# Optimization experiments

Hardware: AMD Instinct MI355X
Metric: run time of the kernel (lower is better)

The kernel has to match this reference:

```python
import jax, jax.numpy as jnp
import numpy as np

TOL_A = 1e-09


def setup_inputs() -> dict:
    key = jax.random.key(0)
    ks = jax.random.split(key, 6)
    nx, nu, ny, bsz, T = 256, 128, 128, 128, 2048
    return {
        "u": jax.random.normal(ks[0], (bsz, T, nu), jnp.float32),
        "M": jax.random.normal(ks[1], (2 * nx, 2 * nx), jnp.float32),
        "B": jax.random.normal(ks[2], (nx, nu), jnp.float32),
        "C": jax.random.normal(ks[3], (ny, nx), jnp.float32),
        "D": jax.random.normal(ks[4], (ny, nu), jnp.float32),
        "x0": jax.random.normal(ks[5], (nx, 1), jnp.float32),
    }


def _compute_A(M):
    # LMI-based stable A: S = M M^T + tol*I; A = E^{-1} F
    nx = M.shape[0] // 2
    S = M @ M.T + TOL_A * jnp.eye(2 * nx, dtype=M.dtype)
    F = S[nx:, :nx]
    P = S[nx:, nx:]
    E = 0.5 * (P + S[:nx, :nx])
    return jnp.linalg.solve(E, F)  # == inv(E) @ F


def reference(u, M, B, C, D, x0):
    # u: (bsz, T, nu); returns predictions (bsz, T, ny)
    nx = B.shape[0]
    A = _compute_A(M)  # time-invariant: computed once instead of per step
    bsz = u.shape[0]
    x = jnp.broadcast_to(x0[:, 0], (bsz, nx))  # learned x0 stacked over batch
    # t=0 output: C x0 + D u_0 (faithful to torch code)
    y0 = x @ C.T + u[:, 0] @ D.T

    def step(x, u_t):
        # x_{t+1} = A x_t + B u_t ; y_{t+1} = C x_{t+1} + D u_t (off-by-one D term, as in source)
        x = x @ A.T + u_t @ B.T
        y = x @ C.T + u_t @ D.T
        return x, y

    # scan over time: xs is (T-1, bsz, nu)
    _, ys = jax.lax.scan(step, x, jnp.swapaxes(u[:, :-1], 0, 1))
    preds = jnp.concatenate([y0[None], ys], axis=0)  # (T, bsz, ny)
    return jnp.swapaxes(preds, 0, 1)
```

## Files before the change

kernel.cpp:

```cpp
#include <hip/hip_runtime.h>

#define NX 256
#define NU 128
#define NY 128
#define BSZ 128
#define TT 2048
#define LCH 32
#define KCH 64

typedef _Float16 h8 __attribute__((ext_vector_type(8)));
typedef _Float16 h4 __attribute__((ext_vector_type(4)));
typedef float f4 __attribute__((ext_vector_type(4)));

__device__ __forceinline__ f4 mfma16(h8 a, h8 b, f4 c) {
  return __builtin_amdgcn_mfma_f32_16x16x32_f16(a, b, c, 0, 0, 0);
}
#define PIN(x) asm volatile("" : "+v"(x))
#define LBAR() asm volatile("s_waitcnt lgkmcnt(0)\n\ts_barrier" ::: "memory")

__device__ __forceinline__ int swz256(int row, int bc) { return row * 256 + (bc ^ ((row & 7) << 4)); }

__device__ __forceinline__ h8 cvt8(f4 lo, f4 hi) {
  h8 h;
#pragma unroll
  for (int j = 0; j < 4; ++j) { h[j] = (_Float16)lo[j]; h[j + 4] = (_Float16)hi[j]; }
  return h;
}
__device__ __forceinline__ h4 h4cvt(f4 v) {
  h4 h;
#pragma unroll
  for (int j = 0; j < 4; ++j) h[j] = (_Float16)v[j];
  return h;
}
__device__ __forceinline__ h8 h8zero() {
  h8 h;
#pragma unroll
  for (int j = 0; j < 8; ++j) h[j] = (_Float16)0.0f;
  return h;
}

__device__ __forceinline__ void mm_core(const float* __restrict__ a, const float* __restrict__ b,
                                        int Nb, int i0, int j0, int tid,
                                        float (*As)[32][65], float (*Bs)[64][33],
                                        float acc[2][2]) {
  const int ar = tid >> 4, ac = (tid & 15) * 4;
  const int br = tid >> 3, bc = (tid & 7) * 4;
  const int tx = tid & 15, ty = tid >> 4;
  f4 pa0 = *(const f4*)(a + (size_t)(i0 + ar) * 256 + ac);
  f4 pa1 = *(const f4*)(a + (size_t)(i0 + ar + 16) * 256 + ac);
  f4 pb0 = *(const f4*)(b + (size_t)br * Nb + j0 + bc);
  f4 pb1 = *(const f4*)(b + (size_t)(br + 32) * Nb + j0 + bc);
  for (int r4 = 0; r4 < 4; ++r4) {
    const int bs = r4 & 1;
#pragma unroll
    for (int m = 0; m < 4; ++m) {
      As[bs][ar][ac + m] = pa0[m];
      As[bs][ar + 16][ac + m] = pa1[m];
      Bs[bs][br][bc + m] = pb0[m];
      Bs[bs][br + 32][bc + m] = pb1[m];
    }
    if (r4 < 3) {
      int kk = (r4 + 1) * 64;
      pa0 = *(const f4*)(a + (size_t)(i0 + ar) * 256 + kk + ac);
      pa1 = *(const f4*)(a + (size_t)(i0 + ar + 16) * 256 + kk + ac);
      pb0 = *(const f4*)(b + (size_t)(kk + br) * Nb + j0 + bc);
      pb1 = *(const f4*)(b + (size_t)(kk + br + 32) * Nb + j0 + bc);
    }
    __syncthreads();
#pragma unroll 8
    for (int k = 0; k < 64; ++k) {
      float a0 = As[bs][ty * 2][k], a1 = As[bs][ty * 2 + 1][k];
      float b0 = Bs[bs][k][tx * 2], b1 = Bs[bs][k][tx * 2 + 1];
      acc[0][0] += a0 * b0; acc[0][1] += a0 * b1;
      acc[1][0] += a1 * b0; acc[1][1] += a1 * b1;
    }
  }
}

__global__ __launch_bounds__(256) void k_ef(const float* __restrict__ M, const float* __restrict__ B,
                                            const float* __restrict__ C, const float* __restrict__ D,
                                            const float* __restrict__ x0, const float* __restrict__ u,
                                            float* __restrict__ E, float* __restrict__ F,
                                            _Float16* __restrict__ B16, float* __restrict__ out) {
  const int tid = threadIdx.x;
  int z = blockIdx.x >> 6;
  if (z >= 2) {
    if (blockIdx.x < 192) {
      int idx = (blockIdx.x - 128) * 256 + tid;
      int b = idx >> 7, col = idx & 127;
      const float* crow = C + (size_t)col * 256;
      const float* drow = D + (size_t)col * 128;
      const float* ur = u + (size_t)b * (TT * NU);
      float s = 0.f;
#pragma unroll 8
      for (int j = 0; j < 256; j += 4) {
        f4 cv = *(const f4*)(crow + j);
        f4 xv = *(const f4*)(x0 + j);
        s += cv[0] * xv[0] + cv[1] * xv[1] + cv[2] * xv[2] + cv[3] * xv[3];
      }
#pragma unroll 8
      for (int j = 0; j < 128; j += 4) {
        f4 dv = *(const f4*)(drow + j);
        f4 uv = *(const f4*)(ur + j);
        s += dv[0] * uv[0] + dv[1] * uv[1] + dv[2] * uv[2] + dv[3] * uv[3];
      }
      out[(size_t)b * (TT * NY) + col] = s;
    } else {
      int i = (blockIdx.x - 192) * 1024 + tid;
      B16[i] = (_Float16)B[i];
      B16[i + 256] = (_Float16)B[i + 256];
      B16[i + 512] = (_Float16)B[i + 512];
      B16[i + 768] = (_Float16)B[i + 768];
    }
    return;
  }
  __shared__ float Ps[2][32][65], Qs[2][32][65];
  int tile = blockIdx.x & 63;
  int i0 = (tile >> 3) * 32, j0 = (tile & 7) * 32;
  const int ar = tid >> 4, ac = (tid & 15) * 4;
  const int tx = tid & 15, ty = tid >> 4;
  float acc[2][2] = {{0.f, 0.f}, {0.f, 0.f}};
  int np = (z == 0) ? 2 : 1;
  int rc = 0;
  for (int p = 0; p < np; ++p) {
    int po = (z == 0) ? p * 256 : 256;
    int qo = (z == 0) ? p * 256 : 0;
    f4 p0 = *(const f4*)(M + (size_t)(i0 + po + ar) * 512 + ac);
    f4 p1 = *(const f4*)(M + (size_t)(i0 + po + ar + 16) * 512 + ac);
    f4 q0 = *(const f4*)(M + (size_t)(j0 + qo + ar) * 512 + ac);
    f4 q1 = *(const f4*)(M + (size_t)(j0 + qo + ar + 16) * 512 + ac);
    for (int kk = 0; kk < 512; kk += 64) {
      const int bs = rc & 1;
      ++rc;
#pragma unroll
      for (int m = 0; m < 4; ++m) {
        Ps[bs][ar][ac + m] = p0[m];
        Ps[bs][ar + 16][ac + m] = p1[m];
        Qs[bs][ar][ac + m] = q0[m];
        Qs[bs][ar + 16][ac + m] = q1[m];
      }
      if (kk < 448) {
        int k2 = kk + 64;
        p0 = *(const f4*)(M + (size_t)(i0 + po + ar) * 512 + k2 + ac);
        p1 = *(const f4*)(M + (size_t)(i0 + po + ar + 16) * 512 + k2 + ac);
        q0 = *(const f4*)(M + (size_t)(j0 + qo + ar) * 512 + k2 + ac);
// ... 55 lines not shown
    }
    red[tid] = s * s;
  }
  __syncthreads();
  for (int o = 128; o > 0; o >>= 1) { if (tid < o) red[tid] += red[tid + o]; __syncthreads(); }
  float c = sqrtf(n1 / red[0]);
  __syncthreads();
  if (blockIdx.x < 64) {
    int i0 = (blockIdx.x >> 3) * 32, j0 = (blockIdx.x & 7) * 32;
    float acc[2][2] = {{0.f, 0.f}, {0.f, 0.f}};
    mm_core(E, E, 256, i0, j0, tid, As, Bs, acc);
    int tx = tid & 15, ty = tid >> 4;
#pragma unroll
    for (int ii = 0; ii < 2; ++ii)
#pragma unroll
      for (int jj = 0; jj < 2; ++jj) {
        int i = i0 + ty * 2 + ii, j = j0 + tx * 2 + jj;
        Y[(size_t)i * 256 + j] = 2.f * c * E[(size_t)i * 256 + j] - c * c * acc[ii][jj];
      }
  } else {
    int idx = (blockIdx.x - 64) * 1024 + tid * 4;
    int i = idx >> 8, j = idx & 255;
    f4 e = *(const f4*)(E + idx);
    f4 v;
#pragma unroll
    for (int m = 0; m < 4; ++m) v[m] = ((j + m) == i ? 2.f * c : 0.f) - c * c * e[m];
    *(f4*)(X + idx) = v;
  }
}

struct MMJob {
  const float* a; const float* b; const float* add;
  float* d32; _Float16* d16;
  int M, N, mode, blk0;
};

__global__ __launch_bounds__(256) void k_mm(MMJob j0, MMJob j1, MMJob j2, int njobs) {
  __shared__ float As[2][32][65];
  __shared__ float Bs[2][64][33];
  const int tid = threadIdx.x;
  int bid = blockIdx.x;
  MMJob jb = j0;
  if (njobs > 1 && bid >= j1.blk0) jb = j1;
  if (njobs > 2 && bid >= j2.blk0) jb = j2;
  int rel = bid - jb.blk0;
  int ntile = jb.N >> 5;
  int i0 = (rel / ntile) * 32, j0g = (rel % ntile) * 32;
  float acc[2][2] = {{0.f, 0.f}, {0.f, 0.f}};
  mm_core(jb.a, jb.b, jb.N, i0, j0g, tid, As, Bs, acc);
  int tx = tid & 15, ty = tid >> 4;
#pragma unroll
  for (int ii = 0; ii < 2; ++ii)
#pragma unroll
    for (int jj = 0; jj < 2; ++jj) {
      int i = i0 + ty * 2 + ii, j = j0g + tx * 2 + jj;
      size_t o = (size_t)i * jb.N + j;
      float v = acc[ii][jj];
      if (jb.mode == 1) v = 2.f * jb.a[(size_t)i * 256 + j] - v;
      else if (jb.add) v += jb.add[o];
      if (jb.d32) jb.d32[o] = v;
      if (jb.d16) jb.d16[o] = (_Float16)v;
    }
}

__global__ __launch_bounds__(512, 2) void k_recW(const float* __restrict__ u,
                                                 const _Float16* __restrict__ A16,
                                                 const _Float16* __restrict__ B16,
                                                 float* __restrict__ w) {
  __shared__ __align__(16) char sm[24576];
  char* xb = sm;
  char* ub = sm + 16384;
  const int tid = threadIdx.x, lane = tid & 63, wv = tid >> 6;
  const int g = lane >> 4, lr = lane & 15;
  const int chunk = blockIdx.x >> 3, btile = blockIdx.x & 7;
  const int b0 = btile * 16, t0 = chunk * LCH, nt0 = wv * 2;

  h8 Ar[2][8], Bf[2][4];
#pragma unroll
  for (int n2 = 0; n2 < 2; ++n2) {
#pragma unroll
    for (int kf = 0; kf < 8; ++kf) {
      Ar[n2][kf] = *(const h8*)(A16 + (size_t)((nt0 + n2) * 16 + lr) * NX + kf * 32 + g * 8);
      PIN(Ar[n2][kf]);
    }
#pragma unroll
    for (int kf = 0; kf < 4; ++kf) {
      Bf[n2][kf] = *(const h8*)(B16 + (size_t)((nt0 + n2) * 16 + lr) * NU + kf * 32 + g * 8);
      PIN(Bf[n2][kf]);
    }
  }
  const int urow = tid >> 5, uuc = tid & 31;
  const float* ubase = u + (size_t)(b0 + urow) * (TT * NU) + uuc * 4;
  const int uoff = swz256(urow, uuc * 8);
  {
    f4 r0 = *(const f4*)(ubase + (size_t)t0 * NU);
    *(h4*)(ub + uoff) = h4cvt(r0);
  }
  f4 urA = *(const f4*)(ubase + (size_t)(t0 + 1) * NU);
  f4 urB = *(const f4*)(ubase + (size_t)(t0 + 2 < TT ? t0 + 2 : TT - 1) * NU);
  h8 af[8];
#pragma unroll
  for (int kf = 0; kf < 8; ++kf) af[kf] = h8zero();
  __syncthreads();

  f4 z4 = {0.f, 0.f, 0.f, 0.f};
  f4 xacc[2];
#pragma unroll 2
  for (int i = 0; i < LCH; ++i) {
    const int p = i & 1;
    if (i < LCH - 1) {
      int nt = t0 + i + 3;
      if (nt > TT - 1) nt = TT - 1;
      if (p == 0) {
        *(h4*)(ub + 4096 + uoff) = h4cvt(urA);
        urA = *(const f4*)(ubase + (size_t)nt * NU);
      } else {
        *(h4*)(ub + uoff) = h4cvt(urB);
        urB = *(const f4*)(ubase + (size_t)nt * NU);
      }
    }
    h8 uf[4];
#pragma unroll
    for (int kf = 0; kf < 4; ++kf)
      uf[kf] = *(const h8*)(ub + p * 4096 + swz256(lr, kf * 64 + g * 16));
    __builtin_amdgcn_s_setprio(1);
    xacc[0] = z4; xacc[1] = z4;
#pragma unroll
    for (int kf = 0; kf < 8; ++kf) {
      xacc[0] = mfma16(Ar[0][kf], af[kf], xacc[0]);
      xacc[1] = mfma16(Ar[1][kf], af[kf], xacc[1]);
    }
#pragma unroll
    for (int kf = 0; kf < 4; ++kf) {
      xacc[0] = mfma16(Bf[0][kf], uf[kf], xacc[0]);
      xacc[1] = mfma16(Bf[1][kf], uf[kf], xacc[1]);
    }
    __builtin_amdgcn_s_setprio(0);
    if (i < LCH - 1) {
#pragma unroll
      for (int n2 = 0; n2 < 2; ++n2)
        *(h4*)(xb + (p ^ 1) * 8192 + lr * 512 + ((((nt0 + n2) * 32) + g * 8) ^ ((lr & 7) << 4))) =
            h4cvt(xacc[n2]);
      LBAR();
#pragma unroll
      for (int kf = 0; kf < 8; ++kf)
        af[kf] = *(const h8*)(xb + (p ^ 1) * 8192 + lr * 512 + ((kf * 64 + g * 16) ^ ((lr & 7) << 4)));
    }
  }
#pragma unroll
  for (int n2 = 0; n2 < 2; ++n2)
    *(f4*)(w + ((size_t)chunk * BSZ + b0 + lr) * NX + (nt0 + n2) * 16 + g * 4) = xacc[n2];
}

__global__ __launch_bounds__(512, 2) void k_phB(const float* __restrict__ x0,
                                                const float* __restrict__ w,
                                                const _Float16* __restrict__ Ah16,
                                                float* __restrict__ xs) {
  __shared__ __align__(16) char xb[16384];
  const int tid = threadIdx.x, lane = tid & 63, wv = tid >> 6;
  const int g = lane >> 4, lr = lane & 15;
  const int b0 = blockIdx.x * 16, nt0 = wv * 2;
  h8 Ar[2][8];
#pragma unroll
  for (int n2 = 0; n2 < 2; ++n2)
#pragma unroll
    for (int kf = 0; kf < 8; ++kf) {
      Ar[n2][kf] = *(const h8*)(Ah16 + (size_t)((nt0 + n2) * 16 + lr) * NX + kf * 32 + g * 8);
      PIN(Ar[n2][kf]);
    }
  for (int s = 0; s < 8; ++s) {
    int e = tid + s * 512;
    int row = e >> 8, c = e & 255;
    xs[(size_t)(b0 + row) * NX + c] = x0[c];
  }
  h8 af[8];
#pragma unroll
  for (int kf = 0; kf < 8; ++kf) {
    const float* sp = x0 + kf * 32 + g * 8;
    af[kf] = cvt8(*(const f4*)sp, *(const f4*)(sp + 4));
  }
  f4 wl[2];
#pragma unroll
  for (int n2 = 0; n2 < 2; ++n2)
    wl[n2] = *(const f4*)(w + ((size_t)0 * BSZ + b0 + lr) * NX + (nt0 + n2) * 16 + g * 4);
// ... 2 lines not shown
    const int p = k & 1;
    f4 wn[2] = {z4, z4};
    if (k < KCH - 2) {
#pragma unroll
      for (int n2 = 0; n2 < 2; ++n2)
        wn[n2] = *(const f4*)(w + ((size_t)(k + 1) * BSZ + b0 + lr) * NX + (nt0 + n2) * 16 + g * 4);
    }
    f4 acc[2] = {z4, z4};
#pragma unroll
    for (int kf = 0; kf < 8; ++kf) {
      acc[0] = mfma16(Ar[0][kf], af[kf], acc[0]);
      acc[1] = mfma16(Ar[1][kf], af[kf], acc[1]);
    }
#pragma unroll
    for (int n2 = 0; n2 < 2; ++n2) {
      acc[n2] += wl[n2];
      *(f4*)(xs + ((size_t)(k + 1) * BSZ + b0 + lr) * NX + (nt0 + n2) * 16 + g * 4) = acc[n2];
    }
    if (k < KCH - 2) {
#pragma unroll
      for (int n2 = 0; n2 < 2; ++n2)
        *(h4*)(xb + (p ^ 1) * 8192 + lr * 512 + ((((nt0 + n2) * 32) + g * 8) ^ ((lr & 7) << 4))) =
            h4cvt(acc[n2]);
      LBAR();
#pragma unroll
      for (int kf = 0; kf < 8; ++kf)
        af[kf] = *(const h8*)(xb + (p ^ 1) * 8192 + lr * 512 + ((kf * 64 + g * 16) ^ ((lr & 7) << 4)));
    }
#pragma unroll
    for (int n2 = 0; n2 < 2; ++n2) wl[n2] = wn[n2];
  }
}

__global__ __launch_bounds__(512, 2) void k_recY(const float* __restrict__ u,
                                                 const _Float16* __restrict__ A16,
                                                 const _Float16* __restrict__ B16,
                                                 const _Float16* __restrict__ CA16,
                                                 const _Float16* __restrict__ CBD16,
                                                 const float* __restrict__ xs,
                                                 float* __restrict__ out) {
  __shared__ __align__(16) char sm[24576];
  char* xb = sm;
  char* ub = sm + 16384;
  const int tid = threadIdx.x, lane = tid & 63, wv = tid >> 6;
  const int g = lane >> 4, lr = lane & 15;
  const int chunk = blockIdx.x >> 3, btile = blockIdx.x & 7;
  const int b0 = btile * 16, t0 = chunk * LCH, nt0 = wv * 2;

  h8 Ar[2][8], Bf[2][4], Cf[8], Df[4];
#pragma unroll
  for (int n2 = 0; n2 < 2; ++n2) {
#pragma unroll
    for (int kf = 0; kf < 8; ++kf) {
      Ar[n2][kf] = *(const h8*)(A16 + (size_t)((nt0 + n2) * 16 + lr) * NX + kf * 32 + g * 8);
      PIN(Ar[n2][kf]);
    }
#pragma unroll
    for (int kf = 0; kf < 4; ++kf) {
      Bf[n2][kf] = *(const h8*)(B16 + (size_t)((nt0 + n2) * 16 + lr) * NU + kf * 32 + g * 8);
      PIN(Bf[n2][kf]);
    }
  }
#pragma unroll
  for (int kf = 0; kf < 8; ++kf) {
    Cf[kf] = *(const h8*)(CA16 + (size_t)(wv * 16 + lr) * NX + kf * 32 + g * 8);
    PIN(Cf[kf]);
  }
#pragma unroll
  for (int kf = 0; kf < 4; ++kf) {
    Df[kf] = *(const h8*)(CBD16 + (size_t)(wv * 16 + lr) * NU + kf * 32 + g * 8);
    PIN(Df[kf]);
  }
  h8 af[8];
#pragma unroll
  for (int kf = 0; kf < 8; ++kf) {
    const float* sp = xs + ((size_t)chunk * BSZ + b0 + lr) * NX + kf * 32 + g * 8;
    af[kf] = cvt8(*(const f4*)sp, *(const f4*)(sp + 4));
  }
  const int urow = tid >> 5, uuc = tid & 31;
  const float* ubase = u + (size_t)(b0 + urow) * (TT * NU) + uuc * 4;
  const int uoff = swz256(urow, uuc * 8);
  float* obase = out + (size_t)(b0 + lr) * (TT * NY) + wv * 16 + g * 4;
  {
    f4 r0 = *(const f4*)(ubase + (size_t)t0 * NU);
    *(h4*)(ub + uoff) = h4cvt(r0);
  }
  f4 urA = *(const f4*)(ubase + (size_t)(t0 + 1) * NU);
  f4 urB = *(const f4*)(ubase + (size_t)(t0 + 2 < TT ? t0 + 2 : TT - 1) * NU);
  __syncthreads();

  f4 z4 = {0.f, 0.f, 0.f, 0.f};
#pragma unroll 2
  for (int i = 0; i < LCH; ++i) {
    const int p = i & 1;
    if (i < LCH - 1) {
      int nt = t0 + i + 3;
      if (nt > TT - 1) nt = TT - 1;
      if (p == 0) {
        *(h4*)(ub + 4096 + uoff) = h4cvt(urA);
        urA = *(const f4*)(ubase + (size_t)nt * NU);
      } else {
        *(h4*)(ub + uoff) = h4cvt(urB);
        urB = *(const f4*)(ubase + (size_t)nt * NU);
      }
    }
    h8 uf[4];
#pragma unroll
    for (int kf = 0; kf < 4; ++kf)
      uf[kf] = *(const h8*)(ub + p * 4096 + swz256(lr, kf * 64 + g * 16));
    if (i < LCH - 1) {
      __builtin_amdgcn_s_setprio(1);
      f4 xacc[2] = {z4, z4};
#pragma unroll
      for (int kf = 0; kf < 8; ++kf) {
        xacc[0] = mfma16(Ar[0][kf], af[kf], xacc[0]);
        xacc[1] = mfma16(Ar[1][kf], af[kf], xacc[1]);
      }
#pragma unroll
      for (int kf = 0; kf < 4; ++kf) {
        xacc[0] = mfma16(Bf[0][kf], uf[kf], xacc[0]);
        xacc[1] = mfma16(Bf[1][kf], uf[kf], xacc[1]);
      }
      __builtin_amdgcn_s_setprio(0);
#pragma unroll
      for (int n2 = 0; n2 < 2; ++n2)
        *(h4*)(xb + (p ^ 1) * 8192 + lr * 512 + ((((nt0 + n2) * 32) + g * 8) ^ ((lr & 7) << 4))) =
            h4cvt(xacc[n2]);
    }
    __builtin_amdgcn_s_setprio(1);
    f4 yacc = z4;
#pragma unroll
    for (int kf = 0; kf < 8; ++kf) yacc = mfma16(Cf[kf], af[kf], yacc);
#pragma unroll
    for (int kf = 0; kf < 4; ++kf) yacc = mfma16(Df[kf], uf[kf], yacc);
    __builtin_amdgcn_s_setprio(0);
    int t = t0 + i + 1;
    if (t < TT) *(f4*)(obase + (size_t)t * NY) = yacc;
    if (i < LCH - 1) {
      LBAR();
#pragma unroll
      for (int kf = 0; kf < 8; ++kf)
        af[kf] = *(const h8*)(xb + (p ^ 1) * 8192 + lr * 512 + ((kf * 64 + g * 16) ^ ((lr & 7) << 4)));
    }
  }
}

extern "C" void kernel_launch(void* const* d_in, const int* in_sizes, int n_in,
                              void* d_out, int out_size, void* d_ws, size_t ws_size,
                              hipStream_t stream) {
  const float* u  = (const float*)d_in[0];
  const float* M  = (const float*)d_in[1];
  const float* B  = (const float*)d_in[2];
  const float* C  = (const float*)d_in[3];
  const float* D  = (const float*)d_in[4];
  const float* x0 = (const float*)d_in[5];
  float* out = (float*)d_out;
  char* ws = (char*)d_ws;

  float* E    = (float*)(ws + 0L);
  float* F    = (float*)(ws + 256L * 1024);
  float* X1   = (float*)(ws + 512L * 1024);
  float* Y1   = (float*)(ws + 768L * 1024);
  float* X2   = (float*)(ws + 1024L * 1024);
  float* Y2   = (float*)(ws + 1280L * 1024);
  float* Amat = (float*)(ws + 1536L * 1024);
  float* P2   = (float*)(ws + 1792L * 1024);
  float* P4   = (float*)(ws + 2048L * 1024);
  float* P8   = (float*)(ws + 2304L * 1024);
  float* P16  = (float*)(ws + 2560L * 1024);
  _Float16* A16   = (_Float16*)(ws + 2816L * 1024);
  _Float16* Ah16  = (_Float16*)(ws + 2944L * 1024);
  _Float16* B16   = (_Float16*)(ws + 3072L * 1024);
  _Float16* CA16  = (_Float16*)(ws + 3136L * 1024);
  _Float16* CBD16 = (_Float16*)(ws + 3200L * 1024);
  float* wbuf = (float*)(ws + 9408L * 1024);
  float* xs   = (float*)(ws + 17600L * 1024);

  MMJob nil = {nullptr, nullptr, nullptr, nullptr, nullptr, 0, 0, 0, 0};

  k_ef<<<224, 256, 0, stream>>>(M, B, C, D, x0, u, E, F, B16, out);
  k_ns0<<<128, 256, 0, stream>>>(E, X1, Y1);
  float *Xc = X1, *Yc = Y1, *Xn = X2, *Yn = Y2;
  for (int it = 0; it < 8; ++it) {
    MMJob jx = {Xc, Yc, nullptr, Xn, nullptr, 256, 256, 1, 0};
    MMJob jy = {Yc, Yc, nullptr, Yn, nullptr, 256, 256, 1, 64};
    k_mm<<<128, 256, 0, stream>>>(jx, jy, nil, 2);
    float* t1 = Xc; Xc = Xn; Xn = t1;
    float* t2 = Yc; Yc = Yn; Yn = t2;
  }
  {
    MMJob ja = {Xc, F, nullptr, Amat, A16, 256, 256, 0, 0};
    k_mm<<<64, 256, 0, stream>>>(ja, nil, nil, 1);
  }
  {
    MMJob j0 = {Amat, Amat, nullptr, P2, nullptr, 256, 256, 0, 0};
    MMJob j1 = {C, Amat, nullptr, nullptr, CA16, 128, 256, 0, 64};
    MMJob j2 = {C, B, D, nullptr, CBD16, 128, 128, 0, 96};
    k_mm<<<112, 256, 0, stream>>>(j0, j1, j2, 3);
  }
  {
    MMJob j0 = {P2, P2, nullptr, P4, nullptr, 256, 256, 0, 0};
    k_mm<<<64, 256, 0, stream>>>(j0, nil, nil, 1);
  }
  {
    MMJob j0 = {P4, P4, nullptr, P8, nullptr, 256, 256, 0, 0};
    k_mm<<<64, 256, 0, stream>>>(j0, nil, nil, 1);
  }
  {
    MMJob j0 = {P8, P8, nullptr, P16, nullptr, 256, 256, 0, 0};
    k_mm<<<64, 256, 0, stream>>>(j0, nil, nil, 1);
  }
  {
    MMJob j0 = {P16, P16, nullptr, nullptr, Ah16, 256, 256, 0, 0};
    k_mm<<<64, 256, 0, stream>>>(j0, nil, nil, 1);
  }

  k_recW<<<512, 512, 0, stream>>>(u, A16, B16, wbuf);
  k_phB<<<8, 512, 0, stream>>>(x0, wbuf, Ah16, xs);
  k_recY<<<512, 512, 0, stream>>>(u, A16, B16, CA16, CBD16, xs, out);
}
```

Measured before the change: 366.4 us.

## Replace serial in-chunk recurrence with precomputed A^k B convolution

```diff
diff --git a/kernel.cpp b/kernel.cpp
--- a/kernel.cpp
+++ b/kernel.cpp
@@ -30,12 +30,6 @@
   h4 h;
 #pragma unroll
   for (int j = 0; j < 4; ++j) h[j] = (_Float16)v[j];
-  return h;
-}
-__device__ __forceinline__ h8 h8zero() {
-  h8 h;
-#pragma unroll
-  for (int j = 0; j < 8; ++j) h[j] = (_Float16)0.0f;
   return h;
 }
 
@@ -81,7 +75,8 @@
                                             const float* __restrict__ C, const float* __restrict__ D,
                                             const float* __restrict__ x0, const float* __restrict__ u,
                                             float* __restrict__ E, float* __restrict__ F,
-                                            _Float16* __restrict__ B16, float* __restrict__ out) {
+                                            _Float16* __restrict__ B16, float* __restrict__ out,
+                                            float* __restrict__ Gs32, _Float16* __restrict__ Gs16) {
   const int tid = threadIdx.x;
   int z = blockIdx.x >> 6;
   if (z >= 2) {
@@ -107,10 +102,14 @@
       out[(size_t)b * (TT * NY) + col] = s;
     } else {
       int i = (blockIdx.x - 192) * 1024 + tid;
-      B16[i] = (_Float16)B[i];
-      B16[i + 256] = (_Float16)B[i + 256];
-      B16[i + 512] = (_Float16)B[i + 512];
-      B16[i + 768] = (_Float16)B[i + 768];
+#pragma unroll
+      for (int s = 0; s < 4; ++s) {
+        int ii = i + s * 256;
+        float v = B[ii];
+        B16[ii] = (_Float16)v;
+        Gs32[ii] = v;
+        Gs16[ii] = (_Float16)v;
+      }
     }
     return;
   }
@@ -232,10 +231,10 @@
 struct MMJob {
   const float* a; const float* b; const float* add;
   float* d32; _Float16* d16;
-  int M, N, mode, blk0;
+  int M, N, mode, blk0, nmat;
 };
 
-__global__ __launch_bounds__(256) void k_mm(MMJob j0, MMJob j1, MMJob j2, int njobs) {
+__global__ __launch_bounds__(256) void k_mm(MMJob j0, MMJob j1, MMJob j2, MMJob j3, int njobs) {
   __shared__ float As[2][32][65];
   __shared__ float Bs[2][64][33];
   const int tid = threadIdx.x;
@@ -243,7 +242,16 @@
   MMJob jb = j0;
   if (njobs > 1 && bid >= j1.blk0) jb = j1;
   if (njobs > 2 && bid >= j2.blk0) jb = j2;
+  if (njobs > 3 && bid >= j3.blk0) jb = j3;
   int rel = bid - jb.blk0;
+  if (jb.nmat > 1) {
+    int tpm = 8 * (jb.N >> 5);
+    int km = rel / tpm;
+    rel -= km * tpm;
+    jb.b += (size_t)km * 32768;
+    if (jb.d32) jb.d32 += (size_t)km * 32768;
+    if (jb.d16) jb.d16 += (size_t)km * 32768;
+  }
   int ntile = jb.N >> 5;
   int i0 = (rel / ntile) * 32, j0g = (rel % ntile) * 32;
   float acc[2][2] = {{0.f, 0.f}, {0.f, 0.f}};
@@ -263,32 +271,14 @@
     }
 }
 
-__global__ __launch_bounds__(512, 2) void k_recW(const float* __restrict__ u,
-                                                 const _Float16* __restrict__ A16,
-                                                 const _Float16* __restrict__ B16,
-                                                 float* __restrict__ w) {
-  __shared__ __align__(16) char sm[24576];
-  char* xb = sm;
-  char* ub = sm + 16384;
+__global__ __launch_bounds__(512, 4) void k_gw(const float* __restrict__ u,
+                                               const _Float16* __restrict__ Gs16,
+                                               float* __restrict__ w) {
+  __shared__ __align__(16) char ub[8192];
   const int tid = threadIdx.x, lane = tid & 63, wv = tid >> 6;
   const int g = lane >> 4, lr = lane & 15;
   const int chunk = blockIdx.x >> 3, btile = blockIdx.x & 7;
   const int b0 = btile * 16, t0 = chunk * LCH, nt0 = wv * 2;
-
-  h8 Ar[2][8], Bf[2][4];
-#pragma unroll
-  for (int n2 = 0; n2 < 2; ++n2) {
-#pragma unroll
-    for (int kf = 0; kf < 8; ++kf) {
-      Ar[n2][kf] = *(const h8*)(A16 + (size_t)((nt0 + n2) * 16 + lr) * NX + kf * 32 + g * 8);
-      PIN(Ar[n2][kf]);
-    }
-#pragma unroll
-    for (int kf = 0; kf < 4; ++kf) {
-      Bf[n2][kf] = *(const h8*)(B16 + (size_t)((nt0 + n2) * 16 + lr) * NU + kf * 32 + g * 8);
-      PIN(Bf[n2][kf]);
-    }
-  }
   const int urow = tid >> 5, uuc = tid & 31;
   const float* ubase = u + (size_t)(b0 + urow) * (TT * NU) + uuc * 4;
   const int uoff = swz256(urow, uuc * 8);
@@ -298,13 +288,21 @@
   }
   f4 urA = *(const f4*)(ubase + (size_t)(t0 + 1) * NU);
   f4 urB = *(const f4*)(ubase + (size_t)(t0 + 2 < TT ? t0 + 2 : TT - 1) * NU);
-  h8 af[8];
-#pragma unroll
-  for (int kf = 0; kf < 8; ++kf) af[kf] = h8zero();
+  const size_t go0 = (size_t)((nt0 + 0) * 16 + lr) * NU + g * 8;
+  const size_t go1 = (size_t)((nt0 + 1) * 16 + lr) * NU + g * 8;
+  h8 Ga[2][4], Gb[2][4];
+  {
+    const _Float16* gp = Gs16 + (size_t)31 * 32768;
+#pragma unroll
+    for (int kf = 0; kf < 4; ++kf) {
+      Ga[0][kf] = *(const h8*)(gp + go0 + kf * 32);
+      Ga[1][kf] = *(const h8*)(gp + go1 + kf * 32);
+    }
+  }
+  f4 z4 = {0.f, 0.f, 0.f, 0.f};
+  f4 xacc[2] = {z4, z4};
   __syncthreads();
 
-  f4 z4 = {0.f, 0.f, 0.f, 0.f};
-  f4 xacc[2];
 #pragma unroll 2
   for (int i = 0; i < LCH; ++i) {
     const int p = i & 1;
@@ -319,33 +317,42 @@
         urB = *(const f4*)(ubase + (size_t)nt * NU);
       }
     }
+    int kn = 30 - i;
+    if (kn < 0) kn = 0;
+    const _Float16* gq = Gs16 + (size_t)kn * 32768;
+    if (p == 0) {
+#pragma unroll
+      for (int kf = 0; kf < 4; ++kf) {
+        Gb[0][kf] = *(const h8*)(gq + go0 + kf * 32);
+        Gb[1][kf] = *(const h8*)(gq + go1 + kf * 32);
+      }
+    } else {
+#pragma unroll
+      for (int kf = 0; kf < 4; ++kf) {
+        Ga[0][kf] = *(const h8*)(gq + go0 + kf * 32);
+        Ga[1][kf] = *(const h8*)(gq + go1 + kf * 32);
+      }
+    }
     h8 uf[4];
 #pragma unroll
     for (int kf = 0; kf < 4; ++kf)
       uf[kf] = *(const h8*)(ub + p * 4096 + swz256(lr, kf * 64 + g * 16));
     __builtin_amdgcn_s_setprio(1);
-    xacc[0] = z4; xacc[1] = z4;
-#pragma unroll
-    for (int kf = 0; kf < 8; ++kf) {
-      xacc[0] = mfma16(Ar[0][kf], af[kf], xacc[0]);
-      xacc[1] = mfma16(Ar[1][kf], af[kf], xacc[1]);
-    }
-#pragma unroll
-    for (int kf = 0; kf < 4; ++kf) {
-      xacc[0] = mfma16(Bf[0][kf], uf[kf], xacc[0]);
-      xacc[1] = mfma16(Bf[1][kf], uf[kf], xacc[1]);
+    if (p == 0) {
+#pragma unroll
+      for (int kf = 0; kf < 4; ++kf) {
+        xacc[0] = mfma16(Ga[0][kf], uf[kf], xacc[0]);
+        xacc[1] = mfma16(Ga[1][kf], uf[kf], xacc[1]);
+      }
+    } else {
+#pragma unroll
+      for (int kf = 0; kf < 4; ++kf) {
+        xacc[0] = mfma16(Gb[0][kf], uf[kf], xacc[0]);
+        xacc[1] = mfma16(Gb[1][kf], uf[kf], xacc[1]);
+      }
     }
     __builtin_amdgcn_s_setprio(0);
-    if (i < LCH - 1) {
-#pragma unroll
-      for (int n2 = 0; n2 < 2; ++n2)
-        *(h4*)(xb + (p ^ 1) * 8192 + lr * 512 + ((((nt0 + n2) * 32) + g * 8) ^ ((lr & 7) << 4))) =
-            h4cvt(xacc[n2]);
-      LBAR();
-#pragma unroll
-      for (int kf = 0; kf < 8; ++kf)
-        af[kf] = *(const h8*)(xb + (p ^ 1) * 8192 + lr * 512 + ((kf * 64 + g * 16) ^ ((lr & 7) << 4)));
-    }
+    if (i < LCH - 1) LBAR();
   }
 #pragma unroll
   for (int n2 = 0; n2 < 2; ++n2)
@@ -559,49 +566,56 @@
   _Float16* B16   = (_Float16*)(ws + 3072L * 1024);
   _Float16* CA16  = (_Float16*)(ws + 3136L * 1024);
   _Float16* CBD16 = (_Float16*)(ws + 3200L * 1024);
+  float* Gs32 = (float*)(ws + 3328L * 1024);
   float* wbuf = (float*)(ws + 9408L * 1024);
   float* xs   = (float*)(ws + 17600L * 1024);
-
-  MMJob nil = {nullptr, nullptr, nullptr, nullptr, nullptr, 0, 0, 0, 0};
-
-  k_ef<<<224, 256, 0, stream>>>(M, B, C, D, x0, u, E, F, B16, out);
+  _Float16* Gs16 = (_Float16*)(ws + 25792L * 1024);
+
+  MMJob nil = {nullptr, nullptr, nullptr, nullptr, nullptr, 0, 0, 0, 0, 1};
+
+  k_ef<<<224, 256, 0, stream>>>(M, B, C, D, x0, u, E, F, B16, out, Gs32, Gs16);
   k_ns0<<<128, 256, 0, stream>>>(E, X1, Y1);
   float *Xc = X1, *Yc = Y1, *Xn = X2, *Yn = Y2;
-  for (int it = 0; it < 8; ++it) {
-    MMJob jx = {Xc, Yc, nullptr, Xn, nullptr, 256, 256, 1, 0};
-    MMJob jy = {Yc, Yc, nullptr, Yn, nullptr, 256, 256, 1, 64};
-    k_mm<<<128, 256, 0, stream>>>(jx, jy, nil, 2);
+  for (int it = 0; it < 6; ++it) {
+    MMJob jx = {Xc, Yc, nullptr, Xn, nullptr, 256, 256, 1, 0, 1};
+    MMJob jy = {Yc, Yc, nullptr, Yn, nullptr, 256, 256, 1, 64, 1};
+    k_mm<<<128, 256, 0, stream>>>(jx, jy, nil, nil, 2);
     float* t1 = Xc; Xc = Xn; Xn = t1;
     float* t2 = Yc; Yc = Yn; Yn = t2;
   }
   {
-    MMJob ja = {Xc, F, nullptr, Amat, A16, 256, 256, 0, 0};
-    k_mm<<<64, 256, 0, stream>>>(ja, nil, nil, 1);
-  }
-  {
-    MMJob j0 = {Amat, Amat, nullptr, P2, nullptr, 256, 256, 0, 0};
-    MMJob j1 = {C, Amat, nullptr, nullptr, CA16, 128, 256, 0, 64};
-    MMJob j2 = {C, B, D, nullptr, CBD16, 128, 128, 0, 96};
-    k_mm<<<112, 256, 0, stream>>>(j0, j1, j2, 3);
-  }
-  {
-    MMJob j0 = {P2, P2, nullptr, P4, nullptr, 256, 256, 0, 0};
-    k_mm<<<64, 256, 0, stream>>>(j0, nil, nil, 1);
-  }
-  {
-    MMJob j0 = {P4, P4, nullptr, P8, nullptr, 256, 256, 0, 0};
-    k_mm<<<64, 256, 0, stream>>>(j0, nil, nil, 1);
-  }
-  {
-    MMJob j0 = {P8, P8, nullptr, P16, nullptr, 256, 256, 0, 0};
-    k_mm<<<64, 256, 0, stream>>>(j0, nil, nil, 1);
-  }
-  {
-    MMJob j0 = {P16, P16, nullptr, nullptr, Ah16, 256, 256, 0, 0};
-    k_mm<<<64, 256, 0, stream>>>(j0, nil, nil, 1);
-  }
-
-  k_recW<<<512, 512, 0, stream>>>(u, A16, B16, wbuf);
+    MMJob ja = {Xc, F, nullptr, Amat, A16, 256, 256, 0, 0, 1};
+    k_mm<<<64, 256, 0, stream>>>(ja, nil, nil, nil, 1);
+  }
+  {
+    MMJob j0 = {Amat, Amat, nullptr, P2, nullptr, 256, 256, 0, 0, 1};
+    MMJob j1 = {Amat, Gs32, nullptr, Gs32 + 32768, Gs16 + 32768, 256, 128, 0, 64, 1};
+    MMJob j2 = {C, Amat, nullptr, nullptr, CA16, 128, 256, 0, 96, 1};
+    MMJob j3 = {C, B, D, nullptr, CBD16, 128, 128, 0, 128, 1};
+    k_mm<<<144, 256, 0, stream>>>(j0, j1, j2, j3, 4);
+  }
+  {
+    MMJob j0 = {P2, P2, nullptr, P4, nullptr, 256, 256, 0, 0, 1};
+    MMJob j1 = {P2, Gs32, nullptr, Gs32 + 2 * 32768, Gs16 + 2 * 32768, 256, 128, 0, 64, 2};
+    k_mm<<<128, 256, 0, stream>>>(j0, j1, nil, nil, 2);
+  }
+  {
+    MMJob j0 = {P4, P4, nullptr, P8, nullptr, 256, 256, 0, 0, 1};
+    MMJob j1 = {P4, Gs32, nullptr, Gs32 + 4 * 32768, Gs16 + 4 * 32768, 256, 128, 0, 64, 4};
+    k_mm<<<192, 256, 0, stream>>>(j0, j1, nil, nil, 2);
+  }
+  {
+    MMJob j0 = {P8, P8, nullptr, P16, nullptr, 256, 256, 0, 0, 1};
+    MMJob j1 = {P8, Gs32, nullptr, Gs32 + 8 * 32768, Gs16 + 8 * 32768, 256, 128, 0, 64, 8};
+    k_mm<<<320, 256, 0, stream>>>(j0, j1, nil, nil, 2);
+  }
+  {
+    MMJob j0 = {P16, P16, nullptr, nullptr, Ah16, 256, 256, 0, 0, 1};
+    MMJob j1 = {P16, Gs32, nullptr, Gs32 + 16 * 32768, Gs16 + 16 * 32768, 256, 128, 0, 64, 16};
+    k_mm<<<576, 256, 0, stream>>>(j0, j1, nil, nil, 2);
+  }
+
+  k_gw<<<512, 512, 0, stream>>>(u, Gs16, wbuf);
   k_phB<<<8, 512, 0, stream>>>(x0, wbuf, Ah16, xs);
   k_recY<<<512, 512, 0, stream>>>(u, A16, B16, CA16, CBD16, xs, out);
 }
```

Measured after the change: 418.8 us. 14.3% more time.

## Interleave two time chunks per block in recurrence kernels and trim Newton-Schulz iterations

Applied to the files above, without the earlier changes.

```diff
diff --git a/kernel.cpp b/kernel.cpp
--- a/kernel.cpp
+++ b/kernel.cpp
@@ -267,13 +267,16 @@
                                                  const _Float16* __restrict__ A16,
                                                  const _Float16* __restrict__ B16,
                                                  float* __restrict__ w) {
-  __shared__ __align__(16) char sm[24576];
-  char* xb = sm;
-  char* ub = sm + 16384;
+  __shared__ __align__(16) char sm[49152];
+  char* xb0 = sm;
+  char* xb1 = sm + 16384;
+  char* ub0 = sm + 32768;
+  char* ub1 = sm + 40960;
   const int tid = threadIdx.x, lane = tid & 63, wv = tid >> 6;
   const int g = lane >> 4, lr = lane & 15;
-  const int chunk = blockIdx.x >> 3, btile = blockIdx.x & 7;
-  const int b0 = btile * 16, t0 = chunk * LCH, nt0 = wv * 2;
+  const int c0 = blockIdx.x >> 3, c1 = c0 + 32, btile = blockIdx.x & 7;
+  const int b0 = btile * 16, nt0 = wv * 2;
+  const int t00 = c0 * LCH, t10 = c1 * LCH;
 
   h8 Ar[2][8], Bf[2][4];
 #pragma unroll
@@ -293,63 +296,85 @@
   const float* ubase = u + (size_t)(b0 + urow) * (TT * NU) + uuc * 4;
   const int uoff = swz256(urow, uuc * 8);
   {
-    f4 r0 = *(const f4*)(ubase + (size_t)t0 * NU);
-    *(h4*)(ub + uoff) = h4cvt(r0);
-  }
-  f4 urA = *(const f4*)(ubase + (size_t)(t0 + 1) * NU);
-  f4 urB = *(const f4*)(ubase + (size_t)(t0 + 2 < TT ? t0 + 2 : TT - 1) * NU);
-  h8 af[8];
-#pragma unroll
-  for (int kf = 0; kf < 8; ++kf) af[kf] = h8zero();
+    f4 r0 = *(const f4*)(ubase + (size_t)t00 * NU);
+    *(h4*)(ub0 + uoff) = h4cvt(r0);
+    f4 r1 = *(const f4*)(ubase + (size_t)t10 * NU);
+    *(h4*)(ub1 + uoff) = h4cvt(r1);
+  }
+  f4 uA0 = *(const f4*)(ubase + (size_t)(t00 + 1) * NU);
+  f4 uB0 = *(const f4*)(ubase + (size_t)(t00 + 2) * NU);
+  f4 uA1 = *(const f4*)(ubase + (size_t)(t10 + 1) * NU);
+  f4 uB1 = *(const f4*)(ubase + (size_t)(t10 + 2 < TT ? t10 + 2 : TT - 1) * NU);
+  h8 af0[8], af1[8];
+#pragma unroll
+  for (int kf = 0; kf < 8; ++kf) { af0[kf] = h8zero(); af1[kf] = h8zero(); }
   __syncthreads();
 
   f4 z4 = {0.f, 0.f, 0.f, 0.f};
-  f4 xacc[2];
+  f4 xc0[2], xc1[2];
 #pragma unroll 2
   for (int i = 0; i < LCH; ++i) {
     const int p = i & 1;
     if (i < LCH - 1) {
-      int nt = t0 + i + 3;
-      if (nt > TT - 1) nt = TT - 1;
+      int n0 = t00 + i + 3;
+      int n1 = t10 + i + 3;
+      if (n1 > TT - 1) n1 = TT - 1;
       if (p == 0) {
-        *(h4*)(ub + 4096 + uoff) = h4cvt(urA);
-        urA = *(const f4*)(ubase + (size_t)nt * NU);
+        *(h4*)(ub0 + 4096 + uoff) = h4cvt(uA0);
+        uA0 = *(const f4*)(ubase + (size_t)n0 * NU);
+        *(h4*)(ub1 + 4096 + uoff) = h4cvt(uA1);
+        uA1 = *(const f4*)(ubase + (size_t)n1 * NU);
       } else {
-        *(h4*)(ub + uoff) = h4cvt(urB);
-        urB = *(const f4*)(ubase + (size_t)nt * NU);
-      }
-    }
-    h8 uf[4];
-#pragma unroll
-    for (int kf = 0; kf < 4; ++kf)
-      uf[kf] = *(const h8*)(ub + p * 4096 + swz256(lr, kf * 64 + g * 16));
+        *(h4*)(ub0 + uoff) = h4cvt(uB0);
+        uB0 = *(const f4*)(ubase + (size_t)n0 * NU);
+        *(h4*)(ub1 + uoff) = h4cvt(uB1);
+        uB1 = *(const f4*)(ubase + (size_t)n1 * NU);
+      }
+    }
+    h8 uf0[4], uf1[4];
+#pragma unroll
+    for (int kf = 0; kf < 4; ++kf) {
+      uf0[kf] = *(const h8*)(ub0 + p * 4096 + swz256(lr, kf * 64 + g * 16));
+      uf1[kf] = *(const h8*)(ub1 + p * 4096 + swz256(lr, kf * 64 + g * 16));
+    }
     __builtin_amdgcn_s_setprio(1);
-    xacc[0] = z4; xacc[1] = z4;
+    xc0[0] = z4; xc0[1] = z4; xc1[0] = z4; xc1[1] = z4;
 #pragma unroll
     for (int kf = 0; kf < 8; ++kf) {
-      xacc[0] = mfma16(Ar[0][kf], af[kf], xacc[0]);
-      xacc[1] = mfma16(Ar[1][kf], af[kf], xacc[1]);
+      xc0[0] = mfma16(Ar[0][kf], af0[kf], xc0[0]);
+      xc1[0] = mfma16(Ar[0][kf], af1[kf], xc1[0]);
+      xc0[1] = mfma16(Ar[1][kf], af0[kf], xc0[1]);
+      xc1[1] = mfma16(Ar[1][kf], af1[kf], xc1[1]);
     }
 #pragma unroll
     for (int kf = 0; kf < 4; ++kf) {
-      xacc[0] = mfma16(Bf[0][kf], uf[kf], xacc[0]);
-      xacc[1] = mfma16(Bf[1][kf], uf[kf], xacc[1]);
+      xc0[0] = mfma16(Bf[0][kf], uf0[kf], xc0[0]);
+      xc1[0] = mfma16(Bf[0][kf], uf1[kf], xc1[0]);
+      xc0[1] = mfma16(Bf[1][kf], uf0[kf], xc0[1]);
+      xc1[1] = mfma16(Bf[1][kf], uf1[kf], xc1[1]);
     }
     __builtin_amdgcn_s_setprio(0);
     if (i < LCH - 1) {
 #pragma unroll
-      for (int n2 = 0; n2 < 2; ++n2)
-        *(h4*)(xb + (p ^ 1) * 8192 + lr * 512 + ((((nt0 + n2) * 32) + g * 8) ^ ((lr & 7) << 4))) =
-            h4cvt(xacc[n2]);
+      for (int n2 = 0; n2 < 2; ++n2) {
+        *(h4*)(xb0 + (p ^ 1) * 8192 + lr * 512 + ((((nt0 + n2) * 32) + g * 8) ^ ((lr & 7) << 4))) =
+            h4cvt(xc0[n2]);
+        *(h4*)(xb1 + (p ^ 1) * 8192 + lr * 512 + ((((nt0 + n2) * 32) + g * 8) ^ ((lr & 7) << 4))) =
+            h4cvt(xc1[n2]);
+      }
       LBAR();
 #pragma unroll
-      for (int kf = 0; kf < 8; ++kf)
-        af[kf] = *(const h8*)(xb + (p ^ 1) * 8192 + lr * 512 + ((kf * 64 + g * 16) ^ ((lr & 7) << 4)));
-    }
-  }
-#pragma unroll
-  for (int n2 = 0; n2 < 2; ++n2)
-    *(f4*)(w + ((size_t)chunk * BSZ + b0 + lr) * NX + (nt0 + n2) * 16 + g * 4) = xacc[n2];
+      for (int kf = 0; kf < 8; ++kf) {
+        af0[kf] = *(const h8*)(xb0 + (p ^ 1) * 8192 + lr * 512 + ((kf * 64 + g * 16) ^ ((lr & 7) << 4)));
+        af1[kf] = *(const h8*)(xb1 + (p ^ 1) * 8192 + lr * 512 + ((kf * 64 + g * 16) ^ ((lr & 7) << 4)));
+      }
+    }
+  }
+#pragma unroll
+  for (int n2 = 0; n2 < 2; ++n2) {
+    *(f4*)(w + ((size_t)c0 * BSZ + b0 + lr) * NX + (nt0 + n2) * 16 + g * 4) = xc0[n2];
+    *(f4*)(w + ((size_t)c1 * BSZ + b0 + lr) * NX + (nt0 + n2) * 16 + g * 4) = xc1[n2];
+  }
 }
 
 __global__ __launch_bounds__(512, 2) void k_phB(const float* __restrict__ x0,
@@ -425,13 +450,16 @@
                                                  const _Float16* __restrict__ CBD16,
                                                  const float* __restrict__ xs,
                                                  float* __restrict__ out) {
-  __shared__ __align__(16) char sm[24576];
-  char* xb = sm;
-  char* ub = sm + 16384;
+  __shared__ __align__(16) char sm[49152];
+  char* xb0 = sm;
+  char* xb1 = sm + 16384;
+  char* ub0 = sm + 32768;
+  char* ub1 = sm + 40960;
   const int tid = threadIdx.x, lane = tid & 63, wv = tid >> 6;
   const int g = lane >> 4, lr = lane & 15;
-  const int chunk = blockIdx.x >> 3, btile = blockIdx.x & 7;
-  const int b0 = btile * 16, t0 = chunk * LCH, nt0 = wv * 2;
+  const int c0 = blockIdx.x >> 3, c1 = c0 + 32, btile = blockIdx.x & 7;
+  const int b0 = btile * 16, nt0 = wv * 2;
+  const int t00 = c0 * LCH, t10 = c1 * LCH;
 
   h8 Ar[2][8], Bf[2][4], Cf[8], Df[4];
 #pragma unroll
@@ -448,31 +476,33 @@
     }
   }
 #pragma unroll
+  for (int kf = 0; kf < 8; ++kf)
+    Cf[kf] = *(const h8*)(CA16 + (size_t)(wv * 16 + lr) * NX + kf * 32 + g * 8);
+#pragma unroll
+  for (int kf = 0; kf < 4; ++kf)
+    Df[kf] = *(const h8*)(CBD16 + (size_t)(wv * 16 + lr) * NU + kf * 32 + g * 8);
+  h8 af0[8], af1[8];
+#pragma unroll
   for (int kf = 0; kf < 8; ++kf) {
-    Cf[kf] = *(const h8*)(CA16 + (size_t)(wv * 16 + lr) * NX + kf * 32 + g * 8);
-    PIN(Cf[kf]);
-  }
-#pragma unroll
-  for (int kf = 0; kf < 4; ++kf) {
-    Df[kf] = *(const h8*)(CBD16 + (size_t)(wv * 16 + lr) * NU + kf * 32 + g * 8);
-    PIN(Df[kf]);
-  }
-  h8 af[8];
-#pragma unroll
-  for (int kf = 0; kf < 8; ++kf) {
-    const float* sp = xs + ((size_t)chunk * BSZ + b0 + lr) * NX + kf * 32 + g * 8;
-    af[kf] = cvt8(*(const f4*)sp, *(const f4*)(sp + 4));
+    const float* s0 = xs + ((size_t)c0 * BSZ + b0 + lr) * NX + kf * 32 + g * 8;
+    af0[kf] = cvt8(*(const f4*)s0, *(const f4*)(s0 + 4));
+    const float* s1 = xs + ((size_t)c1 * BSZ + b0 + lr) * NX + kf * 32 + g * 8;
+    af1[kf] = cvt8(*(const f4*)s1, *(const f4*)(s1 + 4));
   }
   const int urow = tid >> 5, uuc = tid & 31;
   const float* ubase = u + (size_t)(b0 + urow) * (TT * NU) + uuc * 4;
   const int uoff = swz256(urow, uuc * 8);
   float* obase = out + (size_t)(b0 + lr) * (TT * NY) + wv * 16 + g * 4;
   {
-    f4 r0 = *(const f4*)(ubase + (size_t)t0 * NU);
-    *(h4*)(ub + uoff) = h4cvt(r0);
-  }
-  f4 urA = *(const f4*)(ubase + (size_t)(t0 + 1) * NU);
-  f4 urB = *(const f4*)(ubase + (size_t)(t0 + 2 < TT ? t0 + 2 : TT - 1) * NU);
+    f4 r0 = *(const f4*)(ubase + (size_t)t00 * NU);
+    *(h4*)(ub0 + uoff) = h4cvt(r0);
+    f4 r1 = *(const f4*)(ubase + (size_t)t10 * NU);
+    *(h4*)(ub1 + uoff) = h4cvt(r1);
+  }
+  f4 uA0 = *(const f4*)(ubase + (size_t)(t00 + 1) * NU);
+  f4 uB0 = *(const f4*)(ubase + (size_t)(t00 + 2) * NU);
+  f4 uA1 = *(const f4*)(ubase + (size_t)(t10 + 1) * NU);
+  f4 uB1 = *(const f4*)(ubase + (size_t)(t10 + 2 < TT ? t10 + 2 : TT - 1) * NU);
   __syncthreads();
 
   f4 z4 = {0.f, 0.f, 0.f, 0.f};
@@ -480,53 +510,76 @@
   for (int i = 0; i < LCH; ++i) {
     const int p = i & 1;
     if (i < LCH - 1) {
-      int nt = t0 + i + 3;
-      if (nt > TT - 1) nt = TT - 1;
+      int n0 = t00 + i + 3;
+      int n1 = t10 + i + 3;
+      if (n1 > TT - 1) n1 = TT - 1;
       if (p == 0) {
-        *(h4*)(ub + 4096 + uoff) = h4cvt(urA);
-        urA = *(const f4*)(ubase + (size_t)nt * NU);
+        *(h4*)(ub0 + 4096 + uoff) = h4cvt(uA0);
+        uA0 = *(const f4*)(ubase + (size_t)n0 * NU);
+        *(h4*)(ub1 + 4096 + uoff) = h4cvt(uA1);
+        uA1 = *(const f4*)(ubase + (size_t)n1 * NU);
       } else {
-        *(h4*)(ub + uoff) = h4cvt(urB);
-        urB = *(const f4*)(ubase + (size_t)nt * NU);
-      }
-    }
-    h8 uf[4];
-#pragma unroll
-    for (int kf = 0; kf < 4; ++kf)
-      uf[kf] = *(const h8*)(ub + p * 4096 + swz256(lr, kf * 64 + g * 16));
+        *(h4*)(ub0 + uoff) = h4cvt(uB0);
+        uB0 = *(const f4*)(ubase + (size_t)n0 * NU);
+        *(h4*)(ub1 + uoff) = h4cvt(uB1);
+        uB1 = *(const f4*)(ubase + (size_t)n1 * NU);
+      }
+    }
+    h8 uf0[4], uf1[4];
+#pragma unroll
+    for (int kf = 0; kf < 4; ++kf) {
+      uf0[kf] = *(const h8*)(ub0 + p * 4096 + swz256(lr, kf * 64 + g * 16));
+      uf1[kf] = *(const h8*)(ub1 + p * 4096 + swz256(lr, kf * 64 + g * 16));
+    }
     if (i < LCH - 1) {
       __builtin_amdgcn_s_setprio(1);
-      f4 xacc[2] = {z4, z4};
+      f4 xc0[2] = {z4, z4}, xc1[2] = {z4, z4};
 #pragma unroll
       for (int kf = 0; kf < 8; ++kf) {
-        xacc[0] = mfma16(Ar[0][kf], af[kf], xacc[0]);
-        xacc[1] = mfma16(Ar[1][kf], af[kf], xacc[1]);
+        xc0[0] = mfma16(Ar[0][kf], af0[kf], xc0[0]);
+        xc1[0] = mfma16(Ar[0][kf], af1[kf], xc1[0]);
+        xc0[1] = mfma16(Ar[1][kf], af0[kf], xc0[1]);
+        xc1[1] = mfma16(Ar[1][kf], af1[kf], xc1[1]);
       }
 #pragma unroll
       for (int kf = 0; kf < 4; ++kf) {
-        xacc[0] = mfma16(Bf[0][kf], uf[kf], xacc[0]);
-        xacc[1] = mfma16(Bf[1][kf], uf[kf], xacc[1]);
+        xc0[0] = mfma16(Bf[0][kf], uf0[kf], xc0[0]);
+        xc1[0] = mfma16(Bf[0][kf], uf1[kf], xc1[0]);
+        xc0[1] = mfma16(Bf[1][kf], uf0[kf], xc0[1]);
+        xc1[1] = mfma16(Bf[1][kf], uf1[kf], xc1[1]);
       }
       __builtin_amdgcn_s_setprio(0);
 #pragma unroll
-      for (int n2 = 0; n2 < 2; ++n2)
-        *(h4*)(xb + (p ^ 1) * 8192 + lr * 512 + ((((nt0 + n2) * 32) + g * 8) ^ ((lr & 7) << 4))) =
-            h4cvt(xacc[n2]);
+      for (int n2 = 0; n2 < 2; ++n2) {
+        *(h4*)(xb0 + (p ^ 1) * 8192 + lr * 512 + ((((nt0 + n2) * 32) + g * 8) ^ ((lr & 7) << 4))) =
+            h4cvt(xc0[n2]);
+        *(h4*)(xb1 + (p ^ 1) * 8192 + lr * 512 + ((((nt0 + n2) * 32) + g * 8) ^ ((lr & 7) << 4))) =
+            h4cvt(xc1[n2]);
+      }
     }
     __builtin_amdgcn_s_setprio(1);
-    f4 yacc = z4;
-#pragma unroll
-    for (int kf = 0; kf < 8; ++kf) yacc = mfma16(Cf[kf], af[kf], yacc);
-#pragma unroll
-    for (int kf = 0; kf < 4; ++kf) yacc = mfma16(Df[kf], uf[kf], yacc);
+    f4 y0 = z4, y1 = z4;
+#pragma unroll
+    for (int kf = 0; kf < 8; ++kf) {
+      y0 = mfma16(Cf[kf], af0[kf], y0);
+      y1 = mfma16(Cf[kf], af1[kf], y1);
+    }
+#pragma unroll
+    for (int kf = 0; kf < 4; ++kf) {
+      y0 = mfma16(Df[kf], uf0[kf], y0);
+      y1 = mfma16(Df[kf], uf1[kf], y1);
+    }
     __builtin_amdgcn_s_setprio(0);
-    int t = t0 + i + 1;
-    if (t < TT) *(f4*)(obase + (size_t)t * NY) = yacc;
+    int ta = t00 + i + 1, tb = t10 + i + 1;
+    *(f4*)(obase + (size_t)ta * NY) = y0;
+    if (tb < TT) *(f4*)(obase + (size_t)tb * NY) = y1;
     if (i < LCH - 1) {
       LBAR();
 #pragma unroll
-      for (int kf = 0; kf < 8; ++kf)
-        af[kf] = *(const h8*)(xb + (p ^ 1) * 8192 + lr * 512 + ((kf * 64 + g * 16) ^ ((lr & 7) << 4)));
+      for (int kf = 0; kf < 8; ++kf) {
+        af0[kf] = *(const h8*)(xb0 + (p ^ 1) * 8192 + lr * 512 + ((kf * 64 + g * 16) ^ ((lr & 7) << 4)));
+        af1[kf] = *(const h8*)(xb1 + (p ^ 1) * 8192 + lr * 512 + ((kf * 64 + g * 16) ^ ((lr & 7) << 4)));
+      }
     }
   }
 }
@@ -567,7 +620,7 @@
   k_ef<<<224, 256, 0, stream>>>(M, B, C, D, x0, u, E, F, B16, out);
   k_ns0<<<128, 256, 0, stream>>>(E, X1, Y1);
   float *Xc = X1, *Yc = Y1, *Xn = X2, *Yn = Y2;
-  for (int it = 0; it < 8; ++it) {
+  for (int it = 0; it < 6; ++it) {
     MMJob jx = {Xc, Yc, nullptr, Xn, nullptr, 256, 256, 1, 0};
     MMJob jy = {Yc, Yc, nullptr, Yn, nullptr, 256, 256, 1, 64};
     k_mm<<<128, 256, 0, stream>>>(jx, jy, nil, 2);
@@ -601,7 +654,7 @@
     k_mm<<<64, 256, 0, stream>>>(j0, nil, nil, 1);
   }
 
-  k_recW<<<512, 512, 0, stream>>>(u, A16, B16, wbuf);
+  k_recW<<<256, 512, 0, stream>>>(u, A16, B16, wbuf);
   k_phB<<<8, 512, 0, stream>>>(x0, wbuf, Ah16, xs);
-  k_recY<<<512, 512, 0, stream>>>(u, A16, B16, CA16, CBD16, xs, out);
-}
+  k_recY<<<256, 512, 0, stream>>>(u, A16, B16, CA16, CBD16, xs, out);
+}
```

Result: slower. 406.1 us (+10.8%).

## Cache fp16 copy of u in recW and load it directly in recY

Applied to the files above, without the earlier changes.

```diff
diff --git a/kernel.cpp b/kernel.cpp
--- a/kernel.cpp
+++ b/kernel.cpp
@@ -266,7 +266,8 @@
 __global__ __launch_bounds__(512, 2) void k_recW(const float* __restrict__ u,
                                                  const _Float16* __restrict__ A16,
                                                  const _Float16* __restrict__ B16,
-                                                 float* __restrict__ w) {
+                                                 float* __restrict__ w,
+                                                 _Float16* __restrict__ u16o) {
   __shared__ __align__(16) char sm[24576];
   char* xb = sm;
   char* ub = sm + 16384;
@@ -291,10 +292,13 @@
   }
   const int urow = tid >> 5, uuc = tid & 31;
   const float* ubase = u + (size_t)(b0 + urow) * (TT * NU) + uuc * 4;
+  _Float16* u16g = u16o ? (u16o + (size_t)(b0 + urow) * (TT * NU) + uuc * 4) : nullptr;
   const int uoff = swz256(urow, uuc * 8);
   {
     f4 r0 = *(const f4*)(ubase + (size_t)t0 * NU);
-    *(h4*)(ub + uoff) = h4cvt(r0);
+    h4 h0 = h4cvt(r0);
+    *(h4*)(ub + uoff) = h0;
+    if (u16g) *(h4*)(u16g + (size_t)t0 * NU) = h0;
   }
   f4 urA = *(const f4*)(ubase + (size_t)(t0 + 1) * NU);
   f4 urB = *(const f4*)(ubase + (size_t)(t0 + 2 < TT ? t0 + 2 : TT - 1) * NU);
@@ -312,10 +316,14 @@
       int nt = t0 + i + 3;
       if (nt > TT - 1) nt = TT - 1;
       if (p == 0) {
-        *(h4*)(ub + 4096 + uoff) = h4cvt(urA);
+        h4 hh = h4cvt(urA);
+        *(h4*)(ub + 4096 + uoff) = hh;
+        if (u16g) *(h4*)(u16g + (size_t)(t0 + i + 1) * NU) = hh;
         urA = *(const f4*)(ubase + (size_t)nt * NU);
       } else {
-        *(h4*)(ub + uoff) = h4cvt(urB);
+        h4 hh = h4cvt(urB);
+        *(h4*)(ub + uoff) = hh;
+        if (u16g) *(h4*)(u16g + (size_t)(t0 + i + 1) * NU) = hh;
         urB = *(const f4*)(ubase + (size_t)nt * NU);
       }
     }
@@ -418,7 +426,9 @@
   }
 }
 
+template <int DIRECT>
 __global__ __launch_bounds__(512, 2) void k_recY(const float* __restrict__ u,
+                                                 const _Float16* __restrict__ u16,
                                                  const _Float16* __restrict__ A16,
                                                  const _Float16* __restrict__ B16,
                                                  const _Float16* __restrict__ CA16,
@@ -463,37 +473,53 @@
     const float* sp = xs + ((size_t)chunk * BSZ + b0 + lr) * NX + kf * 32 + g * 8;
     af[kf] = cvt8(*(const f4*)sp, *(const f4*)(sp + 4));
   }
+  float* obase = out + (size_t)(b0 + lr) * (TT * NY) + wv * 16 + g * 4;
+
   const int urow = tid >> 5, uuc = tid & 31;
   const float* ubase = u + (size_t)(b0 + urow) * (TT * NU) + uuc * 4;
   const int uoff = swz256(urow, uuc * 8);
-  float* obase = out + (size_t)(b0 + lr) * (TT * NY) + wv * 16 + g * 4;
-  {
+  const _Float16* ub16 = u16 + (size_t)(b0 + lr) * (TT * NU) + g * 8;
+  h8 ufA[4], ufB[4];
+  f4 urA, urB;
+  if constexpr (DIRECT) {
+#pragma unroll
+    for (int kf = 0; kf < 4; ++kf) {
+      ufA[kf] = *(const h8*)(ub16 + (size_t)t0 * NU + kf * 32);
+      ufB[kf] = *(const h8*)(ub16 + (size_t)(t0 + 1) * NU + kf * 32);
+    }
+    __syncthreads();
+  } else {
     f4 r0 = *(const f4*)(ubase + (size_t)t0 * NU);
     *(h4*)(ub + uoff) = h4cvt(r0);
-  }
-  f4 urA = *(const f4*)(ubase + (size_t)(t0 + 1) * NU);
-  f4 urB = *(const f4*)(ubase + (size_t)(t0 + 2 < TT ? t0 + 2 : TT - 1) * NU);
-  __syncthreads();
+    urA = *(const f4*)(ubase + (size_t)(t0 + 1) * NU);
+    urB = *(const f4*)(ubase + (size_t)(t0 + 2 < TT ? t0 + 2 : TT - 1) * NU);
+    __syncthreads();
+  }
 
   f4 z4 = {0.f, 0.f, 0.f, 0.f};
 #pragma unroll 2
   for (int i = 0; i < LCH; ++i) {
     const int p = i & 1;
-    if (i < LCH - 1) {
-      int nt = t0 + i + 3;
-      if (nt > TT - 1) nt = TT - 1;
-      if (p == 0) {
-        *(h4*)(ub + 4096 + uoff) = h4cvt(urA);
-        urA = *(const f4*)(ubase + (size_t)nt * NU);
-      } else {
-        *(h4*)(ub + uoff) = h4cvt(urB);
-        urB = *(const f4*)(ubase + (size_t)nt * NU);
-      }
-    }
     h8 uf[4];
-#pragma unroll
-    for (int kf = 0; kf < 4; ++kf)
-      uf[kf] = *(const h8*)(ub + p * 4096 + swz256(lr, kf * 64 + g * 16));
+    if constexpr (DIRECT) {
+#pragma unroll
+      for (int kf = 0; kf < 4; ++kf) uf[kf] = p ? ufB[kf] : ufA[kf];
+    } else {
+      if (i < LCH - 1) {
+        int nt = t0 + i + 3;
+        if (nt > TT - 1) nt = TT - 1;
+        if (p == 0) {
+          *(h4*)(ub + 4096 + uoff) = h4cvt(urA);
+          urA = *(const f4*)(ubase + (size_t)nt * NU);
+        } else {
+          *(h4*)(ub + uoff) = h4cvt(urB);
+          urB = *(const f4*)(ubase + (size_t)nt * NU);
+        }
+      }
+#pragma unroll
+      for (int kf = 0; kf < 4; ++kf)
+        uf[kf] = *(const h8*)(ub + p * 4096 + swz256(lr, kf * 64 + g * 16));
+    }
     if (i < LCH - 1) {
       __builtin_amdgcn_s_setprio(1);
       f4 xacc[2] = {z4, z4};
@@ -522,6 +548,16 @@
     __builtin_amdgcn_s_setprio(0);
     int t = t0 + i + 1;
     if (t < TT) *(f4*)(obase + (size_t)t * NY) = yacc;
+    if constexpr (DIRECT) {
+      if (i < LCH - 2) {
+        const _Float16* np = ub16 + (size_t)(t0 + i + 2) * NU;
+#pragma unroll
+        for (int kf = 0; kf < 4; ++kf) {
+          if (p) ufB[kf] = *(const h8*)(np + kf * 32);
+          else ufA[kf] = *(const h8*)(np + kf * 32);
+        }
+      }
+    }
     if (i < LCH - 1) {
       LBAR();
 #pragma unroll
@@ -561,13 +597,16 @@
   _Float16* CBD16 = (_Float16*)(ws + 3200L * 1024);
   float* wbuf = (float*)(ws + 9408L * 1024);
   float* xs   = (float*)(ws + 17600L * 1024);
+  const size_t u16_off = 26624L * 1024;
+  bool big = ws_size >= u16_off + (size_t)64 * 1024 * 1024;
+  _Float16* u16 = big ? (_Float16*)(ws + u16_off) : nullptr;
 
   MMJob nil = {nullptr, nullptr, nullptr, nullptr, nullptr, 0, 0, 0, 0};
 
   k_ef<<<224, 256, 0, stream>>>(M, B, C, D, x0, u, E, F, B16, out);
   k_ns0<<<128, 256, 0, stream>>>(E, X1, Y1);
   float *Xc = X1, *Yc = Y1, *Xn = X2, *Yn = Y2;
-  for (int it = 0; it < 8; ++it) {
+  for (int it = 0; it < 6; ++it) {
     MMJob jx = {Xc, Yc, nullptr, Xn, nullptr, 256, 256, 1, 0};
     MMJob jy = {Yc, Yc, nullptr, Yn, nullptr, 256, 256, 1, 64};
     k_mm<<<128, 256, 0, stream>>>(jx, jy, nil, 2);
@@ -601,7 +640,10 @@
     k_mm<<<64, 256, 0, stream>>>(j0, nil, nil, 1);
   }
 
-  k_recW<<<512, 512, 0, stream>>>(u, A16, B16, wbuf);
+  k_recW<<<512, 512, 0, stream>>>(u, A16, B16, wbuf, u16);
   k_phB<<<8, 512, 0, stream>>>(x0, wbuf, Ah16, xs);
-  k_recY<<<512, 512, 0, stream>>>(u, A16, B16, CA16, CBD16, xs, out);
-}
+  if (big)
+    k_recY<1><<<512, 512, 0, stream>>>(u, u16, A16, B16, CA16, CBD16, xs, out);
+  else
+    k_recY<0><<<512, 512, 0, stream>>>(u, u16, A16, B16, CA16, CBD16, xs, out);
+}
```

After: 365.2 us. About the same (-0.3%).
